# Optimization experiments

Hardware: AMD Instinct MI355X
Metric: run time of the kernel (lower is better)

The kernel has to match this reference:

```python
import jax, jax.numpy as jnp
import numpy as np

WS = 32          # window_size -> N = WS*WS = 1024
DIM = 1024
HEADS = 16
BATCH = 16


def _local_mask():
    # token i maps to grid cell (i//WS, i%WS); attend iff within 3x3 neighborhood
    idx = jnp.arange(WS * WS)
    r, c = idx // WS, idx % WS
    return (jnp.abs(r[:, None] - r[None, :]) <= 1) & (jnp.abs(c[:, None] - c[None, :]) <= 1)


def setup_inputs() -> dict:
    key = jax.random.key(0)
    k1, k2, k3 = jax.random.split(key, 3)
    N = WS * WS
    x = jax.random.normal(k1, (BATCH, N, DIM), dtype=jnp.float32)
    w_qkv = jax.random.normal(k2, (3 * DIM, DIM), dtype=jnp.float32) * 0.02
    w_proj = jax.random.normal(k3, (DIM, DIM), dtype=jnp.float32) * 0.02
    b_proj = jnp.zeros((DIM,), dtype=jnp.float32)
    return {"x": x, "w_qkv": w_qkv, "w_proj": w_proj, "b_proj": b_proj}


def reference(x, w_qkv, w_proj, b_proj):
    B, N, C = x.shape
    H = HEADS
    D = C // H
    scale = D ** (-0.5)
    # qkv projection: torch Linear is x @ W^T
    qkv = (x @ w_qkv.T).reshape(B, N, 3, H, D).transpose(2, 0, 3, 1, 4)  # (3,B,H,N,D)
    q, k, v = qkv[0], qkv[1], qkv[2]
    attn = jnp.einsum('bhnd,bhmd->bhnm', q, k) * scale  # (B,H,N,N)
    mask = _local_mask()  # (N,N) bool
    attn = jnp.where(mask[None, None], attn, -jnp.inf)
    attn = jax.nn.softmax(attn, axis=-1)
    out = jnp.einsum('bhnm,bhmd->bhnd', attn, v)          # (B,H,N,D)
    out = out.transpose(0, 2, 1, 3).reshape(B, N, C)      # (B,N,C)
    return out @ w_proj.T + b_proj
```

## Files before the change

### kernel.cpp

```cpp
#include <hip/hip_runtime.h>
#include <hip/hip_bf16.h>
#include <stdint.h>


typedef __bf16 bf16;
typedef __bf16 bf16x4_t __attribute__((ext_vector_type(4)));
typedef __bf16 bf16x8_t __attribute__((ext_vector_type(8)));
typedef float f32x4_t __attribute__((ext_vector_type(4)));

static __device__ __forceinline__ void gload_lds16(const void* g, void* l) {
  __builtin_amdgcn_global_load_lds((__attribute__((address_space(1))) void*)g,
                                   (__attribute__((address_space(3))) void*)l,
                                   16, 0, 0);
}

static __device__ __forceinline__ void block_barrier() {
  asm volatile("" ::: "memory");
  __builtin_amdgcn_s_barrier();
  asm volatile("" ::: "memory");
}

template<int CTRL>
static __device__ __forceinline__ float dpp_xor_add(float v) {
  int x = __builtin_amdgcn_update_dpp(0, __float_as_int(v), CTRL, 0xF, 0xF, true);
  return v + __int_as_float(x);
}

__global__ void cvt_all(const float* __restrict__ x, const float* __restrict__ wq,
                        const float* __restrict__ wp, bf16* __restrict__ xb,
                        bf16* __restrict__ wqb, bf16* __restrict__ wpb) {
  constexpr int NX = 4194304, NWQ = 786432;
  int i = blockIdx.x * blockDim.x + threadIdx.x;
  const float* src; bf16* dst; int off;
  if (i < NX)            { src = x;  dst = xb;  off = i; }
  else if (i < NX + NWQ) { src = wq; dst = wqb; off = i - NX; }
  else                   { src = wp; dst = wpb; off = i - (NX + NWQ); }
  float4 v = reinterpret_cast<const float4*>(src)[off];
  bf16x4_t o;
  o[0] = (bf16)v.x; o[1] = (bf16)v.y; o[2] = (bf16)v.z; o[3] = (bf16)v.w;
  reinterpret_cast<bf16x4_t*>(dst)[off] = o;
}

template<int OUT_BF16>
__global__ __launch_bounds__(512, 2)
void gemm_bk32(const bf16* __restrict__ A, const bf16* __restrict__ Bm,
               void* __restrict__ Cout, const float* __restrict__ bias,
               int M, int N, int K) {
  constexpr int SLOT = 32768;
  extern __shared__ __align__(16) char lds[];

  const int tid = threadIdx.x;
  const int w = tid >> 6, lane = tid & 63;
  const int fr = lane & 15, g = lane >> 4;
  const int wr = w >> 2, wc = w & 3;

  const int nwg = gridDim.x * gridDim.y;
  int lid = blockIdx.y * gridDim.x + blockIdx.x;
  lid = (lid & 7) * (nwg >> 3) + (lid >> 3);
  const int bx = lid % gridDim.x, by = lid / gridDim.x;
  const int row0 = by * 256, col0 = bx * 256;

  const bf16* Ag = A + (size_t)row0 * K;
  const bf16* Bg = Bm + (size_t)col0 * K;
  const int srow = tid >> 2;
  const int scol = ((tid & 3) ^ ((tid >> 3) & 3)) * 8;
  const int nkt  = K >> 5;

  f32x4_t acc[8][4] = {};

  auto stage = [&](int kt, int slot) {
    const int kb = kt << 5;
    char* sb = lds + slot * SLOT;
    gload_lds16(Ag + (size_t)(srow) * K + kb + scol,       sb + tid * 16);
    gload_lds16(Ag + (size_t)(128 + srow) * K + kb + scol, sb + 8192 + tid * 16);
    gload_lds16(Bg + (size_t)(srow) * K + kb + scol,       sb + 16384 + tid * 16);
    gload_lds16(Bg + (size_t)(128 + srow) * K + kb + scol, sb + 24576 + tid * 16);
  };

  const int uxor = ((fr >> 1) & 3) << 4;

  stage(0, 0);
  stage(1, 1);
  asm volatile("s_waitcnt vmcnt(4)" ::: "memory");
  block_barrier();

  for (int kt = 0; kt < nkt; ++kt) {
    const char* cA = lds + (kt & 1) * SLOT;
    const char* cB = cA + 16384;
    const bool pf = (kt + 2 < nkt);

    bf16x8_t a0[4], a1[4], b0[2], b1[2];
    auto lda = [&](bf16x8_t (&dst)[4], int q) {
#pragma unroll
      for (int i = 0; i < 4; ++i) {
        const int row = wr * 128 + (q * 4 + i) * 16 + fr;
        dst[i] = *reinterpret_cast<const bf16x8_t*>(cA + (row << 6) + ((g << 4) ^ uxor));
      }
    };
    auto ldb = [&](bf16x8_t (&dst)[2], int q) {
#pragma unroll
      for (int j = 0; j < 2; ++j) {
        const int row = wc * 64 + (q * 2 + j) * 16 + fr;
        dst[j] = *reinterpret_cast<const bf16x8_t*>(cB + (row << 6) + ((g << 4) ^ uxor));
      }
    };

    lda(a0, 0);
    ldb(b0, 0);
#pragma unroll
    for (int i = 0; i < 4; ++i)
#pragma unroll
      for (int j = 0; j < 2; ++j)
        acc[i][j] = __builtin_amdgcn_mfma_f32_16x16x32_bf16(a0[i], b0[j], acc[i][j], 0, 0, 0);
    ldb(b1, 1);
#pragma unroll
    for (int i = 0; i < 4; ++i)
#pragma unroll
      for (int j = 0; j < 2; ++j)
        acc[i][2 + j] = __builtin_amdgcn_mfma_f32_16x16x32_bf16(a0[i], b1[j], acc[i][2 + j], 0, 0, 0);
    lda(a1, 1);
#pragma unroll
    for (int i = 0; i < 4; ++i)
#pragma unroll
      for (int j = 0; j < 2; ++j)
        acc[4 + i][2 + j] = __builtin_amdgcn_mfma_f32_16x16x32_bf16(
            a1[i], b1[j], acc[4 + i][2 + j], 0, 0, 0);
#pragma unroll
    for (int i = 0; i < 4; ++i)
#pragma unroll
      for (int j = 0; j < 2; ++j)
        acc[4 + i][j] = __builtin_amdgcn_mfma_f32_16x16x32_bf16(
            a1[i], b0[j], acc[4 + i][j], 0, 0, 0);

    block_barrier();
    if (pf) stage(kt + 2, kt & 1);
    if (kt < nkt - 2) asm volatile("s_waitcnt vmcnt(4)" ::: "memory");
    else              asm volatile("s_waitcnt vmcnt(0)" ::: "memory");
    block_barrier();
  }

#pragma unroll
  for (int fm = 0; fm < 8; ++fm) {
    const int rbase = row0 + wr * 128 + fm * 16 + g * 4;
#pragma unroll
    for (int fn = 0; fn < 4; ++fn) {
      const int col = col0 + wc * 64 + fn * 16 + fr;
#pragma unroll
      for (int r = 0; r < 4; ++r) {
        const size_t idx = (size_t)(rbase + r) * N + col;
        if constexpr (OUT_BF16) {
          reinterpret_cast<bf16*>(Cout)[idx] = (bf16)acc[fm][fn][r];
        } else {
          reinterpret_cast<float*>(Cout)[idx] = acc[fm][fn][r] + bias[col];
        }
      }
    }
  }
}

__global__ __launch_bounds__(256)
void local_attn(const bf16* __restrict__ qkv, bf16* __restrict__ outp) {
  __shared__ __align__(16) char sK[12288];
  __shared__ __align__(16) char sV[12288];

  const int tid  = threadIdx.x;
  const int w = tid >> 6, lane = tid & 63;
  const int ch = lane & 7;
  const int bid = blockIdx.x;
  const int r = bid & 31, h = (bid >> 5) & 15, b = bid >> 9;

  const bf16* qkvb = qkv + (size_t)(b * 1024) * 3072 + h * 64;
  const int tokp = w * 8 + (lane >> 3);

#pragma unroll
  for (int u = 0; u < 3; ++u) {
    const int jrow = min(max(r - 1 + u, 0), 31);
    const size_t j = (size_t)(jrow * 32 + tokp);
    gload_lds16(qkvb + j * 3072 + 1024 + ch * 8,
                sK + u * 4096 + w * 1024 + (lane & 7) * 16 + (lane >> 3) * 128);
  }
#pragma unroll
  for (int u = 0; u < 3; ++u) {
    const int jrow = min(max(r - 1 + u, 0), 31);
    const size_t j = (size_t)(jrow * 32 + tokp);
    gload_lds16(qkvb + j * 3072 + 2048 + ch * 8,
                sV + u * 4096 + w * 1024 + (lane & 7) * 16 + (lane >> 3) * 128);
  }

  const int c = tokp, i = r * 32 + c;
  bf16x8_t qv = *reinterpret_cast<const bf16x8_t*>(qkvb + (size_t)i * 3072 + ch * 8);
  float qf[8];
#pragma unroll
  for (int e = 0; e < 8; ++e) qf[e] = (float)qv[e];

  __syncthreads();

  float s[9];
#pragma unroll
  for (int t = 0; t < 9; ++t) {
    const int dr = t / 3 - 1, dc = t % 3 - 1;
    const int rr = r + dr, cc = c + dc;
    const int ccl = min(max(cc, 0), 31);
    const int wtok = (dr + 1) * 32 + ccl;
    const bf16x8_t kvv = *reinterpret_cast<const bf16x8_t*>(sK + wtok * 128 + ch * 16);
    float ps = 0.f;
#pragma unroll
    for (int e = 0; e < 8; ++e) ps += qf[e] * (float)kvv[e];
    ps = dpp_xor_add<0xB1>(ps);
    ps = dpp_xor_add<0x4E>(ps);
    ps += __shfl_xor(ps, 4);
    const bool valid = (rr >= 0 && rr < 32 && cc >= 0 && cc < 32);
    s[t] = ps * 0.125f + (valid ? 0.f : -1e30f);
  }

  float mx = s[0];
#pragma unroll
  for (int t = 1; t < 9; ++t) mx = fmaxf(mx, s[t]);

  float denom = 0.f, o[8] = {};
#pragma unroll
  for (int t = 0; t < 9; ++t) {
    const int dr = t / 3 - 1, dc = t % 3 - 1;
    const int ccl = min(max(c + dc, 0), 31);
    const int wtok = (dr + 1) * 32 + ccl;
    const float p = __expf(s[t] - mx);
    denom += p;
    const bf16x8_t vvv = *reinterpret_cast<const bf16x8_t*>(sV + wtok * 128 + ch * 16);
#pragma unroll
    for (int e = 0; e < 8; ++e) o[e] += p * (float)vvv[e];
  }

  const float inv = 1.f / denom;
  bf16x8_t ov;
#pragma unroll
  for (int e = 0; e < 8; ++e) ov[e] = (bf16)(o[e] * inv);
  *reinterpret_cast<bf16x8_t*>(outp + (size_t)(b * 1024 + i) * 1024 + h * 64 + ch * 8) = ov;
}

extern "C" void kernel_launch(void* const* d_in, const int* in_sizes, int n_in,
                              void* d_out, int out_size, void* d_ws, size_t ws_size,
                              hipStream_t stream) {
  const float* x      = (const float*)d_in[0];
  const float* w_qkv  = (const float*)d_in[1];
  const float* w_proj = (const float*)d_in[2];
  const float* b_proj = (const float*)d_in[3];
  float* out = (float*)d_out;

  const size_t nx   = (size_t)16384 * 1024;
  const size_t nwq  = (size_t)3072 * 1024;
  const size_t nwp  = (size_t)1024 * 1024;
  const size_t nqkv = (size_t)16384 * 3072;

  bf16* x_bf  = (bf16*)d_ws;
  bf16* wq_bf = x_bf + nx;
  bf16* wp_bf = wq_bf + nwq;
  bf16* qkv   = wp_bf + nwp;
  bf16* attn  = qkv + nqkv;

  (void)hipFuncSetAttribute((const void*)&gemm_bk32<1>,
                            hipFuncAttributeMaxDynamicSharedMemorySize, 65536);
  (void)hipFuncSetAttribute((const void*)&gemm_bk32<0>,
                            hipFuncAttributeMaxDynamicSharedMemorySize, 65536);

  cvt_all<<<20480, 256, 0, stream>>>(x, w_qkv, w_proj, x_bf, wq_bf, wp_bf);

  gemm_bk32<1><<<dim3(3072 / 256, 16384 / 256), 512, 65536, stream>>>(
      x_bf, wq_bf, qkv, nullptr, 16384, 3072, 1024);

  local_attn<<<8192, 256, 0, stream>>>(qkv, attn);

  gemm_bk32<0><<<dim3(1024 / 256, 16384 / 256), 512, 65536, stream>>>(
      attn, wp_bf, out, b_proj, 16384, 1024, 1024);
}
```

Measured before the change: 209.0 us.

## Process two query rows per attention block with swizzled LDS and block remap

The local attention kernel now handles two grid rows per block, loading four K/V rows instead of three per row. This cuts the redundant halo loads from 3x to 2x. Each thread now owns 16 head channels instead of 8, which removes one cross-lane shuffle from the reduction. The LDS layout is XOR-swizzled to avoid bank conflicts, and block indices are remapped, likely for XCD locality. Register use goes up and the grid is halved, but the attention kernel is only a small part of total time next to the two GEMMs.

Result: faster. 196.7 us, median of 2 (-5.9%).

```diff
diff --git a/kernel.cpp b/kernel.cpp
--- a/kernel.cpp
+++ b/kernel.cpp
@@ -160,38 +160,37 @@
 
 __global__ __launch_bounds__(256)
 void local_attn(const bf16* __restrict__ qkv, bf16* __restrict__ outp) {
-  __shared__ __align__(16) char sK[12288];
-  __shared__ __align__(16) char sV[12288];
-
-  const int tid  = threadIdx.x;
-  const int w = tid >> 6, lane = tid & 63;
-  const int ch = lane & 7;
-  const int bid = blockIdx.x;
-  const int r = bid & 31, h = (bid >> 5) & 15, b = bid >> 9;
+  __shared__ __align__(16) char sK[16384];
+  __shared__ __align__(16) char sV[16384];
+
+  const int tid = threadIdx.x;
+  int lid = blockIdx.x;
+  lid = (lid & 7) * 512 + (lid >> 3);
+  const int rp = lid & 15, h = (lid >> 4) & 15, b = lid >> 8;
+  const int r0 = rp * 2;
 
   const bf16* qkvb = qkv + (size_t)(b * 1024) * 3072 + h * 64;
-  const int tokp = w * 8 + (lane >> 3);
-
-#pragma unroll
-  for (int u = 0; u < 3; ++u) {
-    const int jrow = min(max(r - 1 + u, 0), 31);
-    const size_t j = (size_t)(jrow * 32 + tokp);
-    gload_lds16(qkvb + j * 3072 + 1024 + ch * 8,
-                sK + u * 4096 + w * 1024 + (lane & 7) * 16 + (lane >> 3) * 128);
-  }
-#pragma unroll
-  for (int u = 0; u < 3; ++u) {
-    const int jrow = min(max(r - 1 + u, 0), 31);
-    const size_t j = (size_t)(jrow * 32 + tokp);
-    gload_lds16(qkvb + j * 3072 + 2048 + ch * 8,
-                sV + u * 4096 + w * 1024 + (lane & 7) * 16 + (lane >> 3) * 128);
-  }
-
-  const int c = tokp, i = r * 32 + c;
-  bf16x8_t qv = *reinterpret_cast<const bf16x8_t*>(qkvb + (size_t)i * 3072 + ch * 8);
-  float qf[8];
-#pragma unroll
-  for (int e = 0; e < 8; ++e) qf[e] = (float)qv[e];
+
+  const int tc = tid >> 3;
+  const int slot = tid & 7;
+  const int unit = slot ^ (tc & 7);
+#pragma unroll
+  for (int p = 0; p < 4; ++p) {
+    const int jrow = min(max(r0 - 1 + p, 0), 31);
+    const bf16* src = qkvb + (size_t)(jrow * 32 + tc) * 3072 + unit * 8;
+    gload_lds16(src + 1024, sK + p * 4096 + tid * 16);
+    gload_lds16(src + 2048, sV + p * 4096 + tid * 16);
+  }
+
+  const int tok = tid >> 2, ch = tid & 3;
+  const int row = r0 + (tok >> 5), col = tok & 31;
+  const int i = row * 32 + col;
+  const bf16* qp = qkvb + (size_t)i * 3072 + ch * 16;
+  bf16x8_t q0 = *reinterpret_cast<const bf16x8_t*>(qp);
+  bf16x8_t q1 = *reinterpret_cast<const bf16x8_t*>(qp + 8);
+  float qf[16];
+#pragma unroll
+  for (int e = 0; e < 8; ++e) { qf[e] = (float)q0[e]; qf[8 + e] = (float)q1[e]; }
 
   __syncthreads();
 
@@ -199,16 +198,20 @@
 #pragma unroll
   for (int t = 0; t < 9; ++t) {
     const int dr = t / 3 - 1, dc = t % 3 - 1;
-    const int rr = r + dr, cc = c + dc;
+    const int rr = row + dr, cc = col + dc;
     const int ccl = min(max(cc, 0), 31);
-    const int wtok = (dr + 1) * 32 + ccl;
-    const bf16x8_t kvv = *reinterpret_cast<const bf16x8_t*>(sK + wtok * 128 + ch * 16);
+    const int wtok = ((tok >> 5) + dr + 1) * 32 + ccl;
+    const int key = ccl & 7;
+    const char* kb = sK + wtok * 128;
+    const bf16x8_t k0 = *reinterpret_cast<const bf16x8_t*>(kb + ((ch * 2) ^ key) * 16);
+    const bf16x8_t k1 = *reinterpret_cast<const bf16x8_t*>(kb + ((ch * 2 + 1) ^ key) * 16);
     float ps = 0.f;
 #pragma unroll
-    for (int e = 0; e < 8; ++e) ps += qf[e] * (float)kvv[e];
+    for (int e = 0; e < 8; ++e) ps += qf[e] * (float)k0[e];
+#pragma unroll
+    for (int e = 0; e < 8; ++e) ps += qf[8 + e] * (float)k1[e];
     ps = dpp_xor_add<0xB1>(ps);
     ps = dpp_xor_add<0x4E>(ps);
-    ps += __shfl_xor(ps, 4);
     const bool valid = (rr >= 0 && rr < 32 && cc >= 0 && cc < 32);
     s[t] = ps * 0.125f + (valid ? 0.f : -1e30f);
   }
@@ -217,24 +220,32 @@
 #pragma unroll
   for (int t = 1; t < 9; ++t) mx = fmaxf(mx, s[t]);
 
-  float denom = 0.f, o[8] = {};
+  float denom = 0.f, o[16] = {};
 #pragma unroll
   for (int t = 0; t < 9; ++t) {
     const int dr = t / 3 - 1, dc = t % 3 - 1;
-    const int ccl = min(max(c + dc, 0), 31);
-    const int wtok = (dr + 1) * 32 + ccl;
+    const int ccl = min(max(col + dc, 0), 31);
+    const int wtok = ((tok >> 5) + dr + 1) * 32 + ccl;
+    const int key = ccl & 7;
     const float p = __expf(s[t] - mx);
     denom += p;
-    const bf16x8_t vvv = *reinterpret_cast<const bf16x8_t*>(sV + wtok * 128 + ch * 16);
-#pragma unroll
-    for (int e = 0; e < 8; ++e) o[e] += p * (float)vvv[e];
+    const char* vb = sV + wtok * 128;
+    const bf16x8_t v0 = *reinterpret_cast<const bf16x8_t*>(vb + ((ch * 2) ^ key) * 16);
+    const bf16x8_t v1 = *reinterpret_cast<const bf16x8_t*>(vb + ((ch * 2 + 1) ^ key) * 16);
+#pragma unroll
+    for (int e = 0; e < 8; ++e) { o[e] += p * (float)v0[e]; o[8 + e] += p * (float)v1[e]; }
   }
 
   const float inv = 1.f / denom;
-  bf16x8_t ov;
-#pragma unroll
-  for (int e = 0; e < 8; ++e) ov[e] = (bf16)(o[e] * inv);
-  *reinterpret_cast<bf16x8_t*>(outp + (size_t)(b * 1024 + i) * 1024 + h * 64 + ch * 8) = ov;
+  bf16x8_t ov0, ov1;
+#pragma unroll
+  for (int e = 0; e < 8; ++e) {
+    ov0[e] = (bf16)(o[e] * inv);
+    ov1[e] = (bf16)(o[8 + e] * inv);
+  }
+  bf16* op = outp + (size_t)(b * 1024 + i) * 1024 + h * 64 + ch * 16;
+  *reinterpret_cast<bf16x8_t*>(op) = ov0;
+  *reinterpret_cast<bf16x8_t*>(op + 8) = ov1;
 }
 
 extern "C" void kernel_launch(void* const* d_in, const int* in_sizes, int n_in,
@@ -267,7 +278,7 @@
   gemm_bk32<1><<<dim3(3072 / 256, 16384 / 256), 512, 65536, stream>>>(
       x_bf, wq_bf, qkv, nullptr, 16384, 3072, 1024);
 
-  local_attn<<<8192, 256, 0, stream>>>(qkv, attn);
+  local_attn<<<4096, 256, 0, stream>>>(qkv, attn);
 
   gemm_bk32<0><<<dim3(1024 / 256, 16384 / 256), 512, 65536, stream>>>(
       attn, wp_bf, out, b_proj, 16384, 1024, 1024);
```
